# Performance work log

Hardware: AMD Instinct MI355X
Metric: run time of the kernel (lower is better)

## Reference

```python
import jax, jax.numpy as jnp
import numpy as np

EPS = 1e-6

def setup_inputs() -> dict:
    key = jax.random.key(0)
    k1, k2 = jax.random.split(key)
    S, B, H, F = 2048, 4, 2048, 8192
    x = jax.random.normal(k1, (S, B, H), dtype=jnp.float32)
    scale = jnp.ones((H,), dtype=jnp.float32)
    ln_bias = jnp.zeros((H,), dtype=jnp.float32)
    kernel = jax.random.normal(k2, (H, F), dtype=jnp.float32) * 0.02  # ~variance_scaling fan_in
    return {"x": x, "scale": scale, "ln_bias": ln_bias, "kernel": kernel}

def reference(x, scale, ln_bias, kernel):
    # LayerNorm over last (hidden) axis, stats in fp32
    mu = jnp.mean(x, axis=-1, keepdims=True)
    var = jnp.mean(jnp.square(x - mu), axis=-1, keepdims=True)
    y = (x - mu) * jax.lax.rsqrt(var + EPS) * scale + ln_bias  # [S,B,H]
    # Dense: contract hidden axis against kernel [H,F]
    z = jnp.einsum('sbh,hf->sbf', y, kernel)  # [S,B,F]
    # return_layernorm_output=True -> (dense_out, ln_out)
    return (z, y)
```

## Files before the change

kernel.cpp:

```cpp
#include <hip/hip_runtime.h>
#include <stdint.h>


typedef __attribute__((ext_vector_type(8))) short short8;
typedef __attribute__((ext_vector_type(4))) float floatx4;

__device__ __forceinline__ unsigned short f2bf(float f) {
    unsigned u = __builtin_bit_cast(unsigned, f);
    u += 0x7fffu + ((u >> 16) & 1u);
    return (unsigned short)(u >> 16);
}

__global__ __launch_bounds__(256) void ln_kernel(
    const float* __restrict__ x, const float* __restrict__ scale,
    const float* __restrict__ bias, float* __restrict__ y,
    unsigned short* __restrict__ ybf, int H)
{
    const int row = blockIdx.x;
    const float* xr = x + (size_t)row * H;
    const int tid = threadIdx.x;

    float4 v0 = ((const float4*)xr)[tid];
    float4 v1 = ((const float4*)xr)[tid + 256];

    float s  = v0.x + v0.y + v0.z + v0.w + v1.x + v1.y + v1.z + v1.w;
    float ss = v0.x*v0.x + v0.y*v0.y + v0.z*v0.z + v0.w*v0.w
             + v1.x*v1.x + v1.y*v1.y + v1.z*v1.z + v1.w*v1.w;

    #pragma unroll
    for (int off = 32; off > 0; off >>= 1) {
        s  += __shfl_down(s,  off, 64);
        ss += __shfl_down(ss, off, 64);
    }
    __shared__ float rs[4], rq[4];
    if ((tid & 63) == 0) { rs[tid >> 6] = s; rq[tid >> 6] = ss; }
    __syncthreads();
    float ts = rs[0] + rs[1] + rs[2] + rs[3];
    float tq = rq[0] + rq[1] + rq[2] + rq[3];
    float mean = ts / (float)H;
    float var  = tq / (float)H - mean * mean;
    float rstd = rsqrtf(var + 1e-6f);

    float4 sc0 = ((const float4*)scale)[tid];
    float4 sc1 = ((const float4*)scale)[tid + 256];
    float4 b0  = ((const float4*)bias)[tid];
    float4 b1  = ((const float4*)bias)[tid + 256];

    float4 o0, o1;
    o0.x = (v0.x - mean) * rstd * sc0.x + b0.x;
    o0.y = (v0.y - mean) * rstd * sc0.y + b0.y;
    o0.z = (v0.z - mean) * rstd * sc0.z + b0.z;
    o0.w = (v0.w - mean) * rstd * sc0.w + b0.w;
    o1.x = (v1.x - mean) * rstd * sc1.x + b1.x;
    o1.y = (v1.y - mean) * rstd * sc1.y + b1.y;
    o1.z = (v1.z - mean) * rstd * sc1.z + b1.z;
    o1.w = (v1.w - mean) * rstd * sc1.w + b1.w;

    float* yr = y + (size_t)row * H;
    ((float4*)yr)[tid]       = o0;
    ((float4*)yr)[tid + 256] = o1;

    unsigned short* br = ybf + (size_t)row * H;
    uint2 p0, p1;
    p0.x = (unsigned)f2bf(o0.x) | ((unsigned)f2bf(o0.y) << 16);
    p0.y = (unsigned)f2bf(o0.z) | ((unsigned)f2bf(o0.w) << 16);
    p1.x = (unsigned)f2bf(o1.x) | ((unsigned)f2bf(o1.y) << 16);
    p1.y = (unsigned)f2bf(o1.z) | ((unsigned)f2bf(o1.w) << 16);
    ((uint2*)br)[tid]       = p0;
    ((uint2*)br)[tid + 256] = p1;
}

__global__ __launch_bounds__(256) void transpose_cast_kernel(
    const float* __restrict__ W, unsigned short* __restrict__ Bt,
    int K, int F)
{
    __shared__ float tile[64][65];
    const int kBase = blockIdx.y * 64;
    const int fBase = blockIdx.x * 64;
    const int tid = threadIdx.x;

    #pragma unroll
    for (int p = 0; p < 4; ++p) {
        int kl = (tid >> 4) + p * 16;
        int fl = (tid & 15) * 4;
        float4 v = *(const float4*)&W[(size_t)(kBase + kl) * F + fBase + fl];
        tile[kl][fl]     = v.x;
        tile[kl][fl + 1] = v.y;
        tile[kl][fl + 2] = v.z;
        tile[kl][fl + 3] = v.w;
    }
    __syncthreads();

    #pragma unroll
    for (int p = 0; p < 2; ++p) {
        int fl = (tid >> 3) + p * 32;
        int k8 = (tid & 7) * 8;
        unsigned w[4];
        #pragma unroll
        for (int j = 0; j < 4; ++j) {
            unsigned lo = f2bf(tile[k8 + 2*j][fl]);
            unsigned hi = f2bf(tile[k8 + 2*j + 1][fl]);
            w[j] = lo | (hi << 16);
        }
        uint4 out = make_uint4(w[0], w[1], w[2], w[3]);
        *(uint4*)&Bt[(size_t)(fBase + fl) * K + kBase + k8] = out;
    }
}

#define GBM 256
#define GBN 256
#define GBK 32

__device__ __forceinline__ void gload16(const unsigned short* src,
                                        unsigned short* dst) {
    __builtin_amdgcn_global_load_lds(
        (const __attribute__((address_space(1))) unsigned int*)src,
        (__attribute__((address_space(3))) unsigned int*)dst, 16, 0, 0);
}

__device__ __forceinline__ void stage_op(
    const unsigned short* __restrict__ g, unsigned short* dst,
    int t, int K, int tid)
{
    #pragma unroll
    for (int i = 0; i < 2; ++i) {
        int e = i * 512 + tid;
        int r = e >> 2;
        int c = (e & 3) ^ ((r >> 1) & 3);
        gload16(g + (size_t)r * K + t * GBK + c * 8, dst + e * 8);
    }
}

__device__ __forceinline__ void read_frags(
    const unsigned short* bufA, const unsigned short* bufB,
    int rowA0, int rowB0, int soff,
    short8 (&a0)[4], short8 (&a1)[4], short8 (&b)[4])
{
    #pragma unroll
    for (int i = 0; i < 4; ++i)
        a0[i] = *(const short8*)(bufA + (rowA0 + i * 16) * 32 + soff);
    #pragma unroll
    for (int j = 0; j < 4; ++j)
        b[j] = *(const short8*)(bufB + (rowB0 + j * 16) * 32 + soff);
    #pragma unroll
    for (int i = 0; i < 4; ++i)
        a1[i] = *(const short8*)(bufA + (rowA0 + 64 + i * 16) * 32 + soff);
}

__device__ __forceinline__ void mfma_tile(
    const short8 (&a0)[4], const short8 (&a1)[4], const short8 (&b)[4],
    floatx4 (&acc)[8][4])
{
    __builtin_amdgcn_s_setprio(1);
    #pragma unroll
    for (int i = 0; i < 4; ++i)
        #pragma unroll
        for (int j = 0; j < 4; ++j)
            acc[i][j] = __builtin_amdgcn_mfma_f32_16x16x32_bf16(
                a0[i], b[j], acc[i][j], 0, 0, 0);
    #pragma unroll
    for (int i = 0; i < 4; ++i)
        #pragma unroll
        for (int j = 0; j < 4; ++j)
            acc[4 + i][j] = __builtin_amdgcn_mfma_f32_16x16x32_bf16(
                a1[i], b[j], acc[4 + i][j], 0, 0, 0);
    __builtin_amdgcn_s_setprio(0);
}

__global__ __launch_bounds__(512, 2) void gemm_bf16_8w(
    const unsigned short* __restrict__ A,
    const unsigned short* __restrict__ Bt,
    float* __restrict__ C,
    int M, int N, int K)
{
    __shared__ __align__(128) unsigned short lds[4][16384];

    const int tid   = threadIdx.x;
    const int lane  = tid & 63;
    const int wave  = tid >> 6;
    const int waveM = wave >> 2;
    const int waveN = wave & 3;
    const int quad  = lane >> 4;
    const int l16   = lane & 15;
    const int soff  = (quad ^ ((l16 >> 1) & 3)) * 8;
    const int rowA0 = waveM * 128 + l16;
    const int rowB0 = waveN * 64 + l16;

    const int nwg = gridDim.x;
    const int cpx = nwg >> 3;
    const int bid = blockIdx.x;
    const int wg  = (bid & 7) * cpx + (bid >> 3);
    const int tilesN = N >> 8;
    const int tm = wg / tilesN;
    const int tn = wg % tilesN;

    const unsigned short* gA = A  + (size_t)tm * GBM * K;
    const unsigned short* gB = Bt + (size_t)tn * GBN * K;

    const int NT = K >> 5;

    floatx4 acc[8][4] = {};
    short8 xa0[4], xa1[4], xb[4];
    short8 ya0[4], ya1[4], yb[4];

    stage_op(gA, &lds[0][0],    0, K, tid);
    stage_op(gB, &lds[0][8192], 0, K, tid);
    stage_op(gA, &lds[1][0],    1, K, tid);
    stage_op(gB, &lds[1][8192], 1, K, tid);
    stage_op(gA, &lds[2][0],    2, K, tid);
    stage_op(gB, &lds[2][8192], 2, K, tid);
    asm volatile("s_waitcnt vmcnt(8)" ::: "memory");
    __builtin_amdgcn_s_barrier();

    for (unsigned t = 0; t < (unsigned)NT; t += 4) {
        {
            int ts = (int)t + 3; if (ts > NT - 1) ts = NT - 1;
            stage_op(gA, &lds[3][0],    ts, K, tid);
            stage_op(gB, &lds[3][8192], ts, K, tid);
            read_frags(&lds[0][0], &lds[0][8192], rowA0, rowB0, soff, xa0, xa1, xb);
            if (t > 0) mfma_tile(ya0, ya1, yb, acc);
            asm volatile("s_waitcnt vmcnt(8) lgkmcnt(0)" ::: "memory");
            __builtin_amdgcn_s_barrier();
        }
        {
            int ts = (int)t + 4; if (ts > NT - 1) ts = NT - 1;
            stage_op(gA, &lds[0][0],    ts, K, tid);
            stage_op(gB, &lds[0][8192], ts, K, tid);
            read_frags(&lds[1][0], &lds[1][8192], rowA0, rowB0, soff, ya0, ya1, yb);
            mfma_tile(xa0, xa1, xb, acc);
            asm volatile("s_waitcnt vmcnt(8) lgkmcnt(0)" ::: "memory");
            __builtin_amdgcn_s_barrier();
        }
        {
            int ts = (int)t + 5; if (ts > NT - 1) ts = NT - 1;
            stage_op(gA, &lds[1][0],    ts, K, tid);
            stage_op(gB, &lds[1][8192], ts, K, tid);
            read_frags(&lds[2][0], &lds[2][8192], rowA0, rowB0, soff, xa0, xa1, xb);
            mfma_tile(ya0, ya1, yb, acc);
            asm volatile("s_waitcnt vmcnt(8) lgkmcnt(0)" ::: "memory");
            __builtin_amdgcn_s_barrier();
        }
        {
            int ts = (int)t + 6; if (ts > NT - 1) ts = NT - 1;
            stage_op(gA, &lds[2][0],    ts, K, tid);
            stage_op(gB, &lds[2][8192], ts, K, tid);
            read_frags(&lds[3][0], &lds[3][8192], rowA0, rowB0, soff, ya0, ya1, yb);
            mfma_tile(xa0, xa1, xb, acc);
            asm volatile("s_waitcnt vmcnt(8) lgkmcnt(0)" ::: "memory");
            __builtin_amdgcn_s_barrier();
        }
    }
    mfma_tile(ya0, ya1, yb, acc);

    const size_t bm = (size_t)tm * GBM;
    const size_t bn = (size_t)tn * GBN;
    #pragma unroll
    for (int mi = 0; mi < 8; ++mi) {
        #pragma unroll
        for (int ni = 0; ni < 4; ++ni) {
            size_t col = bn + (size_t)waveN * 64 + ni * 16 + l16;
            #pragma unroll
            for (int r = 0; r < 4; ++r) {
                size_t row = bm + (size_t)waveM * 128 + mi * 16 + quad * 4 + r;
                C[row * N + col] = acc[mi][ni][r];
            }
        }
    }
}

extern "C" void kernel_launch(void* const* d_in, const int* in_sizes, int n_in,
                              void* d_out, int out_size, void* d_ws, size_t ws_size,
                              hipStream_t stream) {
    const float* x      = (const float*)d_in[0];
    const float* scale  = (const float*)d_in[1];
    const float* lnbias = (const float*)d_in[2];
    const float* W      = (const float*)d_in[3];

    const int H = in_sizes[1];
    const int M = in_sizes[0] / H;
    const int F = in_sizes[3] / H;

    float* z = (float*)d_out;
    float* y = z + (size_t)M * F;

    unsigned short* Abf = (unsigned short*)d_ws;
    unsigned short* Btb = Abf + (size_t)M * H;

    ln_kernel<<<M, 256, 0, stream>>>(x, scale, lnbias, y, Abf, H);
    transpose_cast_kernel<<<dim3(F / 64, H / 64), 256, 0, stream>>>(W, Btb, H, F);
    gemm_bf16_8w<<<dim3((M / GBM) * (F / GBN)), 512, 0, stream>>>(Abf, Btb, z, M, F, H);
}
```

Before: 685.3 us.

## Switch GEMM to 32x32x16 MFMA and add nontemporal loads/stores

The GEMM inner tile now uses 32x32x16 bf16 MFMA instructions with floatx16 accumulators instead of 16x16x32, with new fragment indexing and swizzle offsets plus a rewritten epilogue mapping. This cuts LDS fragment reads per MFMA and raises work per instruction. Separately, the LayerNorm and transpose kernels use nontemporal loads and stores, and the GEMM output uses nontemporal stores to avoid polluting cache. The risk is layout errors in the new fragment mapping and different register pressure.

Measured after the change: 665.7 us. -2.9%, faster.

```diff
diff --git a/kernel.cpp b/kernel.cpp
--- a/kernel.cpp
+++ b/kernel.cpp
@@ -3,7 +3,8 @@
 
 
 typedef __attribute__((ext_vector_type(8))) short short8;
-typedef __attribute__((ext_vector_type(4))) float floatx4;
+typedef __attribute__((ext_vector_type(16))) float floatx16;
+typedef __attribute__((ext_vector_type(4))) float f32x4;
 
 __device__ __forceinline__ unsigned short f2bf(float f) {
     unsigned u = __builtin_bit_cast(unsigned, f);
@@ -20,12 +21,12 @@
     const float* xr = x + (size_t)row * H;
     const int tid = threadIdx.x;
 
-    float4 v0 = ((const float4*)xr)[tid];
-    float4 v1 = ((const float4*)xr)[tid + 256];
-
-    float s  = v0.x + v0.y + v0.z + v0.w + v1.x + v1.y + v1.z + v1.w;
-    float ss = v0.x*v0.x + v0.y*v0.y + v0.z*v0.z + v0.w*v0.w
-             + v1.x*v1.x + v1.y*v1.y + v1.z*v1.z + v1.w*v1.w;
+    f32x4 v0 = __builtin_nontemporal_load((const f32x4*)xr + tid);
+    f32x4 v1 = __builtin_nontemporal_load((const f32x4*)xr + tid + 256);
+
+    float s  = v0[0] + v0[1] + v0[2] + v0[3] + v1[0] + v1[1] + v1[2] + v1[3];
+    float ss = v0[0]*v0[0] + v0[1]*v0[1] + v0[2]*v0[2] + v0[3]*v0[3]
+             + v1[0]*v1[0] + v1[1]*v1[1] + v1[2]*v1[2] + v1[3]*v1[3];
 
     #pragma unroll
     for (int off = 32; off > 0; off >>= 1) {
@@ -41,31 +42,24 @@
     float var  = tq / (float)H - mean * mean;
     float rstd = rsqrtf(var + 1e-6f);
 
-    float4 sc0 = ((const float4*)scale)[tid];
-    float4 sc1 = ((const float4*)scale)[tid + 256];
-    float4 b0  = ((const float4*)bias)[tid];
-    float4 b1  = ((const float4*)bias)[tid + 256];
-
-    float4 o0, o1;
-    o0.x = (v0.x - mean) * rstd * sc0.x + b0.x;
-    o0.y = (v0.y - mean) * rstd * sc0.y + b0.y;
-    o0.z = (v0.z - mean) * rstd * sc0.z + b0.z;
-    o0.w = (v0.w - mean) * rstd * sc0.w + b0.w;
-    o1.x = (v1.x - mean) * rstd * sc1.x + b1.x;
-    o1.y = (v1.y - mean) * rstd * sc1.y + b1.y;
-    o1.z = (v1.z - mean) * rstd * sc1.z + b1.z;
-    o1.w = (v1.w - mean) * rstd * sc1.w + b1.w;
+    f32x4 sc0 = ((const f32x4*)scale)[tid];
+    f32x4 sc1 = ((const f32x4*)scale)[tid + 256];
+    f32x4 b0  = ((const f32x4*)bias)[tid];
+    f32x4 b1  = ((const f32x4*)bias)[tid + 256];
+
+    f32x4 o0 = (v0 - mean) * rstd * sc0 + b0;
+    f32x4 o1 = (v1 - mean) * rstd * sc1 + b1;
 
     float* yr = y + (size_t)row * H;
-    ((float4*)yr)[tid]       = o0;
-    ((float4*)yr)[tid + 256] = o1;
+    __builtin_nontemporal_store(o0, (f32x4*)yr + tid);
+    __builtin_nontemporal_store(o1, (f32x4*)yr + tid + 256);
 
     unsigned short* br = ybf + (size_t)row * H;
     uint2 p0, p1;
-    p0.x = (unsigned)f2bf(o0.x) | ((unsigned)f2bf(o0.y) << 16);
-    p0.y = (unsigned)f2bf(o0.z) | ((unsigned)f2bf(o0.w) << 16);
-    p1.x = (unsigned)f2bf(o1.x) | ((unsigned)f2bf(o1.y) << 16);
-    p1.y = (unsigned)f2bf(o1.z) | ((unsigned)f2bf(o1.w) << 16);
+    p0.x = (unsigned)f2bf(o0[0]) | ((unsigned)f2bf(o0[1]) << 16);
+    p0.y = (unsigned)f2bf(o0[2]) | ((unsigned)f2bf(o0[3]) << 16);
+    p1.x = (unsigned)f2bf(o1[0]) | ((unsigned)f2bf(o1[1]) << 16);
+    p1.y = (unsigned)f2bf(o1[2]) | ((unsigned)f2bf(o1[3]) << 16);
     ((uint2*)br)[tid]       = p0;
     ((uint2*)br)[tid + 256] = p1;
 }
@@ -83,11 +77,12 @@
     for (int p = 0; p < 4; ++p) {
         int kl = (tid >> 4) + p * 16;
         int fl = (tid & 15) * 4;
-        float4 v = *(const float4*)&W[(size_t)(kBase + kl) * F + fBase + fl];
-        tile[kl][fl]     = v.x;
-        tile[kl][fl + 1] = v.y;
-        tile[kl][fl + 2] = v.z;
-        tile[kl][fl + 3] = v.w;
+        f32x4 v = __builtin_nontemporal_load(
+            (const f32x4*)&W[(size_t)(kBase + kl) * F + fBase + fl]);
+        tile[kl][fl]     = v[0];
+        tile[kl][fl + 1] = v[1];
+        tile[kl][fl + 2] = v[2];
+        tile[kl][fl + 3] = v[3];
     }
     __syncthreads();
 
@@ -131,39 +126,38 @@
     }
 }
 
-__device__ __forceinline__ void read_frags(
+__device__ __forceinline__ void read_frags32(
     const unsigned short* bufA, const unsigned short* bufB,
-    int rowA0, int rowB0, int soff,
-    short8 (&a0)[4], short8 (&a1)[4], short8 (&b)[4])
-{
-    #pragma unroll
-    for (int i = 0; i < 4; ++i)
-        a0[i] = *(const short8*)(bufA + (rowA0 + i * 16) * 32 + soff);
-    #pragma unroll
-    for (int j = 0; j < 4; ++j)
-        b[j] = *(const short8*)(bufB + (rowB0 + j * 16) * 32 + soff);
-    #pragma unroll
-    for (int i = 0; i < 4; ++i)
-        a1[i] = *(const short8*)(bufA + (rowA0 + 64 + i * 16) * 32 + soff);
-}
-
-__device__ __forceinline__ void mfma_tile(
-    const short8 (&a0)[4], const short8 (&a1)[4], const short8 (&b)[4],
-    floatx4 (&acc)[8][4])
+    int rA, int rB, int s0a, int s1a,
+    short8 (&a)[4][2], short8 (&b)[2][2])
+{
+    #pragma unroll
+    for (int rb = 0; rb < 4; ++rb) {
+        const unsigned short* rp = bufA + (rA + rb * 32) * 32;
+        a[rb][0] = *(const short8*)(rp + s0a);
+        a[rb][1] = *(const short8*)(rp + s1a);
+    }
+    #pragma unroll
+    for (int cb = 0; cb < 2; ++cb) {
+        const unsigned short* rp = bufB + (rB + cb * 32) * 32;
+        b[cb][0] = *(const short8*)(rp + s0a);
+        b[cb][1] = *(const short8*)(rp + s1a);
+    }
+}
+
+__device__ __forceinline__ void mfma_tile32(
+    const short8 (&a)[4][2], const short8 (&b)[2][2], floatx16 (&acc)[4][2])
 {
     __builtin_amdgcn_s_setprio(1);
     #pragma unroll
-    for (int i = 0; i < 4; ++i)
+    for (int rb = 0; rb < 4; ++rb)
         #pragma unroll
-        for (int j = 0; j < 4; ++j)
-            acc[i][j] = __builtin_amdgcn_mfma_f32_16x16x32_bf16(
-                a0[i], b[j], acc[i][j], 0, 0, 0);
-    #pragma unroll
-    for (int i = 0; i < 4; ++i)
-        #pragma unroll
-        for (int j = 0; j < 4; ++j)
-            acc[4 + i][j] = __builtin_amdgcn_mfma_f32_16x16x32_bf16(
-                a1[i], b[j], acc[4 + i][j], 0, 0, 0);
+        for (int cb = 0; cb < 2; ++cb) {
+            acc[rb][cb] = __builtin_amdgcn_mfma_f32_32x32x16_bf16(
+                a[rb][0], b[cb][0], acc[rb][cb], 0, 0, 0);
+            acc[rb][cb] = __builtin_amdgcn_mfma_f32_32x32x16_bf16(
+                a[rb][1], b[cb][1], acc[rb][cb], 0, 0, 0);
+        }
     __builtin_amdgcn_s_setprio(0);
 }
 
@@ -180,11 +174,13 @@
     const int wave  = tid >> 6;
     const int waveM = wave >> 2;
     const int waveN = wave & 3;
-    const int quad  = lane >> 4;
-    const int l16   = lane & 15;
-    const int soff  = (quad ^ ((l16 >> 1) & 3)) * 8;
-    const int rowA0 = waveM * 128 + l16;
-    const int rowB0 = waveN * 64 + l16;
+    const int l31   = lane & 31;
+    const int lhi   = lane >> 5;
+    const int xsw   = (l31 >> 1) & 3;
+    const int s0a   = ((0 + lhi) ^ xsw) * 8;
+    const int s1a   = ((2 + lhi) ^ xsw) * 8;
+    const int rA    = waveM * 128 + l31;
+    const int rB    = waveN * 64 + l31;
 
     const int nwg = gridDim.x;
     const int cpx = nwg >> 3;
@@ -199,9 +195,9 @@
 
     const int NT = K >> 5;
 
-    floatx4 acc[8][4] = {};
-    short8 xa0[4], xa1[4], xb[4];
-    short8 ya0[4], ya1[4], yb[4];
+    floatx16 acc[4][2] = {};
+    short8 xa[4][2], xb[2][2];
+    short8 ya[4][2], yb[2][2];
 
     stage_op(gA, &lds[0][0],    0, K, tid);
     stage_op(gB, &lds[0][8192], 0, K, tid);
@@ -217,8 +213,8 @@
             int ts = (int)t + 3; if (ts > NT - 1) ts = NT - 1;
             stage_op(gA, &lds[3][0],    ts, K, tid);
             stage_op(gB, &lds[3][8192], ts, K, tid);
-            read_frags(&lds[0][0], &lds[0][8192], rowA0, rowB0, soff, xa0, xa1, xb);
-            if (t > 0) mfma_tile(ya0, ya1, yb, acc);
+            read_frags32(&lds[0][0], &lds[0][8192], rA, rB, s0a, s1a, xa, xb);
+            if (t > 0) mfma_tile32(ya, yb, acc);
             asm volatile("s_waitcnt vmcnt(8) lgkmcnt(0)" ::: "memory");
             __builtin_amdgcn_s_barrier();
         }
@@ -226,8 +222,8 @@
             int ts = (int)t + 4; if (ts > NT - 1) ts = NT - 1;
             stage_op(gA, &lds[0][0],    ts, K, tid);
             stage_op(gB, &lds[0][8192], ts, K, tid);
-            read_frags(&lds[1][0], &lds[1][8192], rowA0, rowB0, soff, ya0, ya1, yb);
-            mfma_tile(xa0, xa1, xb, acc);
+            read_frags32(&lds[1][0], &lds[1][8192], rA, rB, s0a, s1a, ya, yb);
+            mfma_tile32(xa, xb, acc);
             asm volatile("s_waitcnt vmcnt(8) lgkmcnt(0)" ::: "memory");
             __builtin_amdgcn_s_barrier();
         }
@@ -235,8 +231,8 @@
             int ts = (int)t + 5; if (ts > NT - 1) ts = NT - 1;
             stage_op(gA, &lds[1][0],    ts, K, tid);
             stage_op(gB, &lds[1][8192], ts, K, tid);
-            read_frags(&lds[2][0], &lds[2][8192], rowA0, rowB0, soff, xa0, xa1, xb);
-            mfma_tile(ya0, ya1, yb, acc);
+            read_frags32(&lds[2][0], &lds[2][8192], rA, rB, s0a, s1a, xa, xb);
+            mfma_tile32(ya, yb, acc);
             asm volatile("s_waitcnt vmcnt(8) lgkmcnt(0)" ::: "memory");
             __builtin_amdgcn_s_barrier();
         }
@@ -244,25 +240,26 @@
             int ts = (int)t + 6; if (ts > NT - 1) ts = NT - 1;
             stage_op(gA, &lds[2][0],    ts, K, tid);
             stage_op(gB, &lds[2][8192], ts, K, tid);
-            read_frags(&lds[3][0], &lds[3][8192], rowA0, rowB0, soff, ya0, ya1, yb);
-            mfma_tile(xa0, xa1, xb, acc);
-            asm volatile("s_waitcnt vmcnt(8) lgkmcnt(0)" ::: "memory");
-            __builtin_amdgcn_s_barrier();
-        }
-    }
-    mfma_tile(ya0, ya1, yb, acc);
+            read_frags32(&lds[3][0], &lds[3][8192], rA, rB, s0a, s1a, ya, yb);
+            mfma_tile32(xa, xb, acc);
+            asm volatile("s_waitcnt vmcnt(8) lgkmcnt(0)" ::: "memory");
+            __builtin_amdgcn_s_barrier();
+        }
+    }
+    mfma_tile32(ya, yb, acc);
 
     const size_t bm = (size_t)tm * GBM;
     const size_t bn = (size_t)tn * GBN;
     #pragma unroll
-    for (int mi = 0; mi < 8; ++mi) {
+    for (int rb = 0; rb < 4; ++rb) {
         #pragma unroll
-        for (int ni = 0; ni < 4; ++ni) {
-            size_t col = bn + (size_t)waveN * 64 + ni * 16 + l16;
+        for (int cb = 0; cb < 2; ++cb) {
+            size_t col = bn + (size_t)waveN * 64 + cb * 32 + l31;
             #pragma unroll
-            for (int r = 0; r < 4; ++r) {
-                size_t row = bm + (size_t)waveM * 128 + mi * 16 + quad * 4 + r;
-                C[row * N + col] = acc[mi][ni][r];
+            for (int i = 0; i < 16; ++i) {
+                size_t row = bm + (size_t)waveM * 128 + rb * 32
+                           + (i & 3) + 8 * (i >> 2) + 4 * lhi;
+                __builtin_nontemporal_store(acc[rb][cb][i], &C[row * N + col]);
             }
         }
     }
```
